# Optimization experiments

Measured on AMD Instinct MI355X. Metric: run time of the kernel, lower is better.

Reference implementation:

```python
import jax, jax.numpy as jnp
import numpy as np
from jax import lax

N = 8388608
NG = 1024
TAU = 0.1
GAMMA = 0.05
MAX_ITERS = 30
EPS = 1e-9


def setup_inputs() -> dict:
    key = jax.random.key(0)
    k1, k2, k3 = jax.random.split(key, 3)
    y_raw = jax.random.uniform(k1, (N,), dtype=jnp.float32)
    y_real = jax.random.uniform(k2, (N,), dtype=jnp.float32)
    group_ids = jax.random.randint(k3, (N,), 0, NG, dtype=jnp.int32)
    return {"y_raw": y_raw, "y_real": y_real, "group_ids": group_ids, "n_groups": NG}


def reference(y_raw, y_real, group_ids, n_groups):
    y_real = jnp.maximum(y_real, EPS)
    l = (1.0 - TAU) * y_real          # per-element lower box bound
    u = (1.0 + TAU) * y_real          # per-element upper box bound
    y_clipped = jnp.clip(y_raw, l, u)
    w = 1.0 / jnp.maximum(y_real, 1e-9)

    seg_sum = lambda v: jax.ops.segment_sum(v, group_ids, num_segments=n_groups)

    n_g = seg_sum(jnp.ones_like(y_raw))            # [G] group sizes
    L = (1.0 - GAMMA) * n_g
    U = (1.0 + GAMMA) * n_g
    S0 = seg_sum(w * y_clipped)                    # [G] ratio sums at alpha=0
    feasible = (S0 >= L) & (S0 <= U)

    # per-group bracketing interval for alpha
    alo = jax.ops.segment_min((l - y_raw) * w, group_ids, num_segments=n_groups) - 1.0
    ahi = jax.ops.segment_max((u - y_raw) * w, group_ids, num_segments=n_groups) + 1.0
    nonempty = n_g > 0
    alo = jnp.where(nonempty, alo, 0.0)            # guard empty groups (inf/-inf)
    ahi = jnp.where(nonempty, ahi, 0.0)
    T = jnp.where(S0 < L, L, U)                    # [G] bisection target

    def step(carry, _):
        lo, hi, _ = carry
        mid = 0.5 * (lo + hi)                                    # [G]
        y_mid = jnp.clip(y_raw + mid[group_ids] / w, l, u)       # [N]
        Smid = seg_sum(w * y_mid)                                # [G]
        lo = jnp.where(Smid < T, mid, lo)
        hi = jnp.where(Smid >= T, mid, hi)
        return (lo, hi, mid), None

    (lo, hi, mid), _ = lax.scan(step, (alo, ahi, alo), None, length=MAX_ITERS)
    y_bis = jnp.clip(y_raw + mid[group_ids] / w, l, u)           # last iterate y_mid
    return jnp.where(feasible[group_ids], y_clipped, y_bis)
```

## Files before the change

kernel.cpp:

```cpp
#include <hip/hip_runtime.h>

#define NGROUPS  1024
#define EPSF     1e-9f
#define MAX_ITERS 30
#define CNT_SHIFT 18
#define SUM_MASK  0x3FFFFu
#define QSCALE    128.0f
#define QINV      (1.0f / 128.0f)
#define SBLK 512
#define PTILE 2
#define NPASS 4
#define PERBLK (SBLK * PTILE * NPASS)
#define NSHADOW 8

typedef float vfloat4 __attribute__((ext_vector_type(4)));

__device__ __forceinline__ unsigned enc_f(float f) {
    unsigned u = __float_as_uint(f);
    return (u & 0x80000000u) ? ~u : (u | 0x80000000u);
}
__device__ __forceinline__ float dec_f(unsigned e) {
    unsigned u = (e & 0x80000000u) ? (e ^ 0x80000000u) : ~e;
    return __uint_as_float(u);
}

__global__ __launch_bounds__(NGROUPS) void k_init(unsigned* gpack) {
#pragma unroll
    for (int c = 0; c < NSHADOW; ++c) gpack[c * NGROUPS + threadIdx.x] = 0u;
}

__device__ __forceinline__ void stats4(float4 yr, float4 ye, int4 gg,
                                       unsigned* s_pk, float4* __restrict__ out4,
                                       int idx) {
    float yrs[4] = { yr.x, yr.y, yr.z, yr.w };
    float yes[4] = { ye.x, ye.y, ye.z, ye.w };
    int   gs[4]  = { gg.x, gg.y, gg.z, gg.w };
    float oc[4];
#pragma unroll
    for (int j = 0; j < 4; ++j) {
        float yraw = yrs[j];
        float yrc  = fmaxf(yes[j], EPSF);
        float l = 0.9f * yrc;
        float u = 1.1f * yrc;
        float yclip = fminf(fmaxf(yraw, l), u);
        oc[j] = yclip;
        float s = yclip / yrc;
        unsigned pk = (1u << CNT_SHIFT)
                    + __float2uint_rn((s - 0.9f) * QSCALE);
        atomicAdd(&s_pk[gs[j]], pk);
    }
    vfloat4 o = { oc[0], oc[1], oc[2], oc[3] };
    __builtin_nontemporal_store(o, (vfloat4*)&out4[idx]);
}

__device__ __forceinline__ void loadp(const float4* __restrict__ yraw4,
                                      const float4* __restrict__ yreal4,
                                      const int4*   __restrict__ gid4,
                                      int b, float4* yr, float4* ye, int4* gg) {
#pragma unroll
    for (int k = 0; k < PTILE; ++k) yr[k] = yraw4[b + k * SBLK];
#pragma unroll
    for (int k = 0; k < PTILE; ++k) ye[k] = yreal4[b + k * SBLK];
#pragma unroll
    for (int k = 0; k < PTILE; ++k) gg[k] = gid4[b + k * SBLK];
}
__device__ __forceinline__ void compp(const float4* yr, const float4* ye,
                                      const int4* gg, unsigned* s_pk,
                                      float4* __restrict__ out4, int b) {
#pragma unroll
    for (int k = 0; k < PTILE; ++k)
        stats4(yr[k], ye[k], gg[k], s_pk, out4, b + k * SBLK);
}

template <bool EXACT>
__global__ __launch_bounds__(SBLK, 4) void k_stats(const float4* __restrict__ yraw4,
                                                   const float4* __restrict__ yreal4,
                                                   const int4*   __restrict__ gid4,
                                                   float4*       __restrict__ out4,
                                                   unsigned* gpack, int n4) {
    __shared__ unsigned s_pk[NGROUPS];
    int t = threadIdx.x;
    int base = blockIdx.x * PERBLK + t;

    if (EXACT) {
        float4 yr0[PTILE], ye0[PTILE]; int4 gg0[PTILE];
        float4 yr1[PTILE], ye1[PTILE]; int4 gg1[PTILE];
        float4 yr2[PTILE], ye2[PTILE]; int4 gg2[PTILE];
        float4 yr3[PTILE], ye3[PTILE]; int4 gg3[PTILE];
        const int st = SBLK * PTILE;
        int b0 = base, b1 = base + st, b2 = base + 2 * st, b3 = base + 3 * st;

        loadp(yraw4, yreal4, gid4, b0, yr0, ye0, gg0);
        s_pk[t] = 0u; s_pk[t + SBLK] = 0u;
        __syncthreads();
        loadp(yraw4, yreal4, gid4, b1, yr1, ye1, gg1);
        compp(yr0, ye0, gg0, s_pk, out4, b0);
        loadp(yraw4, yreal4, gid4, b2, yr2, ye2, gg2);
        compp(yr1, ye1, gg1, s_pk, out4, b1);
        loadp(yraw4, yreal4, gid4, b3, yr3, ye3, gg3);
        compp(yr2, ye2, gg2, s_pk, out4, b2);
        compp(yr3, ye3, gg3, s_pk, out4, b3);
    } else {
        s_pk[t] = 0u; s_pk[t + SBLK] = 0u;
        __syncthreads();
#pragma unroll
        for (int k = 0; k < PTILE * NPASS; ++k) {
            int i = base + k * SBLK;
            if (i >= n4) continue;
            float4 a = yraw4[i], b = yreal4[i];
            int4 g4 = gid4[i];
            stats4(a, b, g4, s_pk, out4, i);
        }
    }
    __syncthreads();
    unsigned v0 = s_pk[t], v1 = s_pk[t + SBLK];
    unsigned* gp = gpack + (blockIdx.x & (NSHADOW - 1)) * NGROUPS;
    if (v0) atomicAdd(&gp[t], v0);
    if (v1) atomicAdd(&gp[t + SBLK], v1);
}

__global__ __launch_bounds__(NGROUPS) void k_group(const unsigned* gpack,
                                                   unsigned* feas, float* gT,
                                                   unsigned* gmn, unsigned* gmx,
                                                   unsigned* gbase, unsigned* gcur,
                                                   unsigned* gcnt, unsigned* total) {
    __shared__ unsigned s_scan[NGROUPS];
    int g = threadIdx.x;
    unsigned c = 0u, q = 0u;
#pragma unroll
    for (int s = 0; s < NSHADOW; ++s) {
        unsigned pk = gpack[s * NGROUPS + g];
        c += pk >> CNT_SHIFT;
        q += pk & SUM_MASK;
    }
    float nf = (float)c;
    float S0 = 0.9f * nf + (float)q * QINV;
    float L = 0.95f * nf;
    float U = 1.05f * nf;
    unsigned f = (S0 >= L && S0 <= U) ? 1u : 0u;
    feas[g] = f;
    gT[g]   = (S0 < L) ? L : U;
    gcnt[g] = c;
    gmn[g]  = 0xFFFFFFFFu;
    gmx[g]  = 0u;

    unsigned v = f ? 0u : c;
    s_scan[g] = v;
    for (int off = 1; off < NGROUPS; off <<= 1) {
        __syncthreads();
        unsigned tmp = (g >= off) ? s_scan[g - off] : 0u;
        __syncthreads();
        s_scan[g] += tmp;
    }
    __syncthreads();
    unsigned incl = s_scan[g];
    unsigned base = incl - v;
    gbase[g] = base;
    gcur[g]  = base;
    if (g == NGROUPS - 1) *total = incl;
}

__global__ __launch_bounds__(256) void k_mmc(const float4* __restrict__ yraw4,
                                             const float4* __restrict__ yreal4,
                                             const int4*   __restrict__ gid4,
                                             const unsigned* __restrict__ feas,
                                             unsigned* gcur, const unsigned* total,
                                             unsigned* gmn, unsigned* gmx,
                                             unsigned* cidx, unsigned* cgid,
                                             unsigned capacity, int n4) {
    if (*total == 0u) return;
    __shared__ unsigned s_feas[NGROUPS];
    __shared__ unsigned s_mn[NGROUPS];
    __shared__ unsigned s_mx[NGROUPS];
    for (int g = threadIdx.x; g < NGROUPS; g += blockDim.x) {
        s_feas[g] = feas[g]; s_mn[g] = 0xFFFFFFFFu; s_mx[g] = 0u;
    }
    __syncthreads();
    int stride = gridDim.x * blockDim.x;
    for (int i = blockIdx.x * blockDim.x + threadIdx.x; i < n4; i += stride) {
        int4 gg = gid4[i];
        int gs[4] = { gg.x, gg.y, gg.z, gg.w };
        bool any = !s_feas[gs[0]] || !s_feas[gs[1]] || !s_feas[gs[2]] || !s_feas[gs[3]];
        if (!any) continue;
        float4 yr = yraw4[i];
        float4 ye = yreal4[i];
        float yrs[4] = { yr.x, yr.y, yr.z, yr.w };
        float yes[4] = { ye.x, ye.y, ye.z, ye.w };
#pragma unroll
        for (int j = 0; j < 4; ++j) {
            int g = gs[j];
            if (s_feas[g]) continue;
            float yraw = yrs[j];
            float yrc  = fmaxf(yes[j], EPSF);
            float l = 0.9f * yrc;
            float u = 1.1f * yrc;
            float w = 1.0f / yrc;
            float a0 = (l - yraw) * w;
            float a1 = (u - yraw) * w;
            atomicMin(&s_mn[g], enc_f(a0));
            atomicMax(&s_mx[g], enc_f(a1));
            unsigned pos = atomicAdd(&gcur[g], 1u);
            if (pos < capacity) {
                cidx[pos] = (unsigned)(4 * i + j);
                cgid[pos] = (unsigned)g;
            }
        }
    }
    __syncthreads();
    for (int g = threadIdx.x; g < NGROUPS; g += blockDim.x) {
        if (!s_feas[g]) {
            atomicMin(&gmn[g], s_mn[g]);
            atomicMax(&gmx[g], s_mx[g]);
        }
    }
}

#define CAPC 8064
__global__ __launch_bounds__(256) void k_bisect(const float* __restrict__ y_raw,
                                                const float* __restrict__ y_real,
                                                const unsigned* feas,
                                                const unsigned* gcnt,
                                                const unsigned* gbase, const float* gT,
                                                const unsigned* gmn, const unsigned* gmx,
                                                const unsigned* __restrict__ cidx,
                                                float* __restrict__ out,
                                                unsigned capacity) {
    int g = blockIdx.x;
    if (feas[g]) return;
    __shared__ float2 cache[CAPC];
    __shared__ double s_part[4];
    __shared__ float  s_mid;
    unsigned base = gbase[g];
    unsigned cnt  = gcnt[g];
    if (base >= capacity) cnt = 0;
    else if (cnt > capacity - base) cnt = capacity - base;
    int t = threadIdx.x;
    for (unsigned i = t; i < cnt && i < CAPC; i += 256u) {
        unsigned idx = cidx[base + i];
        cache[i] = make_float2(y_raw[idx], y_real[idx]);
    }
    __syncthreads();
    float lo = dec_f(gmn[g]) - 1.0f;
    float hi = dec_f(gmx[g]) + 1.0f;
    float T  = gT[g];
    for (int it = 0; it < MAX_ITERS; ++it) {
        if (t == 0) s_mid = 0.5f * (lo + hi);
        __syncthreads();
        float m = s_mid;
        double part = 0.0;
        for (unsigned i = t; i < cnt; i += 256u) {
            float yraw, ye;
            if (i < CAPC) { float2 v = cache[i]; yraw = v.x; ye = v.y; }
            else { unsigned idx = cidx[base + i]; yraw = y_raw[idx]; ye = y_real[idx]; }
            float yrc = fmaxf(ye, EPSF);
            float l = 0.9f * yrc;
            float u = 1.1f * yrc;
            float w = 1.0f / yrc;
            float ym = fminf(fmaxf(yraw + m / w, l), u);
            part += (double)(w * ym);
        }
#pragma unroll
        for (int off = 32; off > 0; off >>= 1) part += __shfl_down(part, off, 64);
        if ((t & 63) == 0) s_part[t >> 6] = part;
        __syncthreads();
        if (t == 0) {
            float Smid = (float)(s_part[0] + s_part[1] + s_part[2] + s_part[3]);
            if (Smid < T) lo = m; else hi = m;
        }
        __syncthreads();
    }
    float m = s_mid;
    for (unsigned i = t; i < cnt; i += 256u) {
        unsigned idx = cidx[base + i];
        float yraw, ye;
        if (i < CAPC) { float2 v = cache[i]; yraw = v.x; ye = v.y; }
        else { yraw = y_raw[idx]; ye = y_real[idx]; }
        float yrc = fmaxf(ye, EPSF);
        float l = 0.9f * yrc;
        float u = 1.1f * yrc;
        float w = 1.0f / yrc;
        out[idx] = fminf(fmaxf(yraw + m / w, l), u);
    }
}

extern "C" void kernel_launch(void* const* d_in, const int* in_sizes, int n_in,
                              void* d_out, int out_size, void* d_ws, size_t ws_size,
                              hipStream_t stream) {
    const float* y_raw  = (const float*)d_in[0];
    const float* y_real = (const float*)d_in[1];
    const int*   gid    = (const int*)d_in[2];
    float* out = (float*)d_out;
    const int n  = in_sizes[0];
    const int n4 = n / 4;

    char* ws = (char*)d_ws;
    unsigned* gpack  = (unsigned*)(ws + 0);
    unsigned* gmn    = (unsigned*)(ws + 32768);
    unsigned* gmx    = (unsigned*)(ws + 36864);
    unsigned* feas   = (unsigned*)(ws + 40960);
    float*    gT     = (float*)(ws + 45056);
    unsigned* gbase  = (unsigned*)(ws + 49152);
    unsigned* gcur   = (unsigned*)(ws + 53248);
    unsigned* gcnt   = (unsigned*)(ws + 57344);
    unsigned* total  = (unsigned*)(ws + 61440);
    unsigned* cidx   = (unsigned*)(ws + 65536);
    size_t cap64 = (ws_size > 65536) ? (ws_size - 65536) / 8 : 0;
    if (cap64 > (size_t)n) cap64 = (size_t)n;
    unsigned capacity = (unsigned)cap64;
    unsigned* cgid = cidx + capacity;

    k_init<<<1, NGROUPS, 0, stream>>>(gpack);
    if (n4 % PERBLK == 0) {
        k_stats<true><<<n4 / PERBLK, SBLK, 0, stream>>>(
            (const float4*)y_raw, (const float4*)y_real, (const int4*)gid,
            (float4*)out, gpack, n4);
    } else {
        k_stats<false><<<(n4 + PERBLK - 1) / PERBLK, SBLK, 0, stream>>>(
            (const float4*)y_raw, (const float4*)y_real, (const int4*)gid,
            (float4*)out, gpack, n4);
    }
    k_group<<<1, NGROUPS, 0, stream>>>(gpack, feas, gT, gmn, gmx, gbase, gcur,
                                       gcnt, total);
    k_mmc<<<512, 256, 0, stream>>>((const float4*)y_raw, (const float4*)y_real,
                                   (const int4*)gid, feas, gcur, total,
                                   gmn, gmx, cidx, cgid, capacity, n4);
    k_bisect<<<NGROUPS, 256, 0, stream>>>(y_raw, y_real, feas, gcnt, gbase, gT,
                                          gmn, gmx, cidx, out, capacity);
}
```

Before: 142.6 us.

## Shrink stats blocks, widen shadow histograms, flush with 64-bit paired atomics

```diff
diff --git a/kernel.cpp b/kernel.cpp
--- a/kernel.cpp
+++ b/kernel.cpp
@@ -9,9 +9,8 @@
 #define QINV      (1.0f / 128.0f)
 #define SBLK 512
 #define PTILE 2
-#define NPASS 4
-#define PERBLK (SBLK * PTILE * NPASS)
-#define NSHADOW 8
+#define PERBLK (SBLK * PTILE)
+#define NSHADOW 32
 
 typedef float vfloat4 __attribute__((ext_vector_type(4)));
 
@@ -53,27 +52,8 @@
     __builtin_nontemporal_store(o, (vfloat4*)&out4[idx]);
 }
 
-__device__ __forceinline__ void loadp(const float4* __restrict__ yraw4,
-                                      const float4* __restrict__ yreal4,
-                                      const int4*   __restrict__ gid4,
-                                      int b, float4* yr, float4* ye, int4* gg) {
-#pragma unroll
-    for (int k = 0; k < PTILE; ++k) yr[k] = yraw4[b + k * SBLK];
-#pragma unroll
-    for (int k = 0; k < PTILE; ++k) ye[k] = yreal4[b + k * SBLK];
-#pragma unroll
-    for (int k = 0; k < PTILE; ++k) gg[k] = gid4[b + k * SBLK];
-}
-__device__ __forceinline__ void compp(const float4* yr, const float4* ye,
-                                      const int4* gg, unsigned* s_pk,
-                                      float4* __restrict__ out4, int b) {
-#pragma unroll
-    for (int k = 0; k < PTILE; ++k)
-        stats4(yr[k], ye[k], gg[k], s_pk, out4, b + k * SBLK);
-}
-
 template <bool EXACT>
-__global__ __launch_bounds__(SBLK, 4) void k_stats(const float4* __restrict__ yraw4,
+__global__ __launch_bounds__(SBLK, 8) void k_stats(const float4* __restrict__ yraw4,
                                                    const float4* __restrict__ yreal4,
                                                    const int4*   __restrict__ gid4,
                                                    float4*       __restrict__ out4,
@@ -83,28 +63,22 @@
     int base = blockIdx.x * PERBLK + t;
 
     if (EXACT) {
-        float4 yr0[PTILE], ye0[PTILE]; int4 gg0[PTILE];
-        float4 yr1[PTILE], ye1[PTILE]; int4 gg1[PTILE];
-        float4 yr2[PTILE], ye2[PTILE]; int4 gg2[PTILE];
-        float4 yr3[PTILE], ye3[PTILE]; int4 gg3[PTILE];
-        const int st = SBLK * PTILE;
-        int b0 = base, b1 = base + st, b2 = base + 2 * st, b3 = base + 3 * st;
-
-        loadp(yraw4, yreal4, gid4, b0, yr0, ye0, gg0);
+        float4 yr0, yr1, ye0, ye1;
+        int4   gg0, gg1;
+        yr0 = yraw4[base];            yr1 = yraw4[base + SBLK];
+        ye0 = yreal4[base];           ye1 = yreal4[base + SBLK];
+        gg0 = gid4[base];             gg1 = gid4[base + SBLK];
+
         s_pk[t] = 0u; s_pk[t + SBLK] = 0u;
         __syncthreads();
-        loadp(yraw4, yreal4, gid4, b1, yr1, ye1, gg1);
-        compp(yr0, ye0, gg0, s_pk, out4, b0);
-        loadp(yraw4, yreal4, gid4, b2, yr2, ye2, gg2);
-        compp(yr1, ye1, gg1, s_pk, out4, b1);
-        loadp(yraw4, yreal4, gid4, b3, yr3, ye3, gg3);
-        compp(yr2, ye2, gg2, s_pk, out4, b2);
-        compp(yr3, ye3, gg3, s_pk, out4, b3);
+
+        stats4(yr0, ye0, gg0, s_pk, out4, base);
+        stats4(yr1, ye1, gg1, s_pk, out4, base + SBLK);
     } else {
         s_pk[t] = 0u; s_pk[t + SBLK] = 0u;
         __syncthreads();
 #pragma unroll
-        for (int k = 0; k < PTILE * NPASS; ++k) {
+        for (int k = 0; k < PTILE; ++k) {
             int i = base + k * SBLK;
             if (i >= n4) continue;
             float4 a = yraw4[i], b = yreal4[i];
@@ -113,10 +87,12 @@
         }
     }
     __syncthreads();
-    unsigned v0 = s_pk[t], v1 = s_pk[t + SBLK];
-    unsigned* gp = gpack + (blockIdx.x & (NSHADOW - 1)) * NGROUPS;
-    if (v0) atomicAdd(&gp[t], v0);
-    if (v1) atomicAdd(&gp[t + SBLK], v1);
+    unsigned lo = s_pk[2 * t], hi = s_pk[2 * t + 1];
+    if (lo | hi) {
+        unsigned* gp = gpack + (blockIdx.x & (NSHADOW - 1)) * NGROUPS;
+        unsigned long long pair = ((unsigned long long)hi << 32) | (unsigned long long)lo;
+        atomicAdd((unsigned long long*)&gp[2 * t], pair);
+    }
 }
 
 __global__ __launch_bounds__(NGROUPS) void k_group(const unsigned* gpack,
@@ -295,16 +271,16 @@
 
     char* ws = (char*)d_ws;
     unsigned* gpack  = (unsigned*)(ws + 0);
-    unsigned* gmn    = (unsigned*)(ws + 32768);
-    unsigned* gmx    = (unsigned*)(ws + 36864);
-    unsigned* feas   = (unsigned*)(ws + 40960);
-    float*    gT     = (float*)(ws + 45056);
-    unsigned* gbase  = (unsigned*)(ws + 49152);
-    unsigned* gcur   = (unsigned*)(ws + 53248);
-    unsigned* gcnt   = (unsigned*)(ws + 57344);
-    unsigned* total  = (unsigned*)(ws + 61440);
-    unsigned* cidx   = (unsigned*)(ws + 65536);
-    size_t cap64 = (ws_size > 65536) ? (ws_size - 65536) / 8 : 0;
+    unsigned* gmn    = (unsigned*)(ws + 131072);
+    unsigned* gmx    = (unsigned*)(ws + 135168);
+    unsigned* feas   = (unsigned*)(ws + 139264);
+    float*    gT     = (float*)(ws + 143360);
+    unsigned* gbase  = (unsigned*)(ws + 147456);
+    unsigned* gcur   = (unsigned*)(ws + 151552);
+    unsigned* gcnt   = (unsigned*)(ws + 155648);
+    unsigned* total  = (unsigned*)(ws + 159744);
+    unsigned* cidx   = (unsigned*)(ws + 163840);
+    size_t cap64 = (ws_size > 163840) ? (ws_size - 163840) / 8 : 0;
     if (cap64 > (size_t)n) cap64 = (size_t)n;
     unsigned capacity = (unsigned)cap64;
     unsigned* cgid = cidx + capacity;
```

After: 143.3 us. No clear change (+0.5%).
